# Kernel tuning notes

Measured on AMD Instinct MI355X. Metric: run time of the kernel, lower is better.

Reference implementation:

```python
import jax, jax.numpy as jnp
import numpy as np

D_MODEL = 1024  # scaling uses sqrt(d_model), as in the source


def setup_inputs() -> dict:
    key = jax.random.key(0)
    kx, kq, kk, kv = jax.random.split(key, 4)
    B, N, D, H = 4, 4096, D_MODEL, 128
    X = jax.random.normal(kx, (B, N, D), dtype=jnp.float32)
    # nn.Linear(d_model, d_head, bias=False) weights, stored as [d_model, d_head]
    s = 1.0 / np.sqrt(D)
    Wq = jax.random.normal(kq, (D, H), dtype=jnp.float32) * s
    Wk = jax.random.normal(kk, (D, H), dtype=jnp.float32) * s
    Wv = jax.random.normal(kv, (D, H), dtype=jnp.float32) * s
    return {"X": X, "Wq": Wq, "Wk": Wk, "Wv": Wv}


def reference(X, Wq, Wk, Wv):
    # Q, K, V: [B, N, H]
    Q = jnp.einsum("bnd,dh->bnh", X, Wq)
    K = jnp.einsum("bnd,dh->bnh", X, Wk)
    V = jnp.einsum("bnd,dh->bnh", X, Wv)
    # Scores: [B, N, N]; source divides by sqrt(d_model) (not sqrt(d_head))
    A = jnp.einsum("bqh,bkh->bqk", Q, K) / jnp.sqrt(jnp.float32(D_MODEL))
    A = jax.nn.softmax(A, axis=-1)
    # Dropout is identity in eval mode (deterministic reference baseline)
    return jnp.einsum("bqk,bkh->bqh", A, V)
```

## Files before the change

### kernel.cpp

```cpp
#include <hip/hip_runtime.h>
#include <stdint.h>

typedef __bf16 bf16_t;
typedef bf16_t bf16x8 __attribute__((ext_vector_type(8)));
typedef float f32x4 __attribute__((ext_vector_type(4)));
typedef float f32x16 __attribute__((ext_vector_type(16)));
typedef unsigned short u16;
typedef unsigned int u32;

#define MFMA16(a, b, c) __builtin_amdgcn_mfma_f32_16x16x32_bf16((a), (b), (c), 0, 0, 0)
#define MFMA32(a, b, c) __builtin_amdgcn_mfma_f32_32x32x16_bf16((a), (b), (c), 0, 0, 0)

#define QSCALE 0.04508422002778633f

__device__ __forceinline__ u16 f2bf(float f) {
  union { float f; unsigned u; } v; v.f = f;
  unsigned r = v.u + 0x7fffu + ((v.u >> 16) & 1u);
  return (u16)(r >> 16);
}

__device__ __forceinline__ float exp2x(float x) {
#if __has_builtin(__builtin_amdgcn_exp2f)
  return __builtin_amdgcn_exp2f(x);
#else
  return exp2f(x);
#endif
}

__device__ __forceinline__ float rcpx(float x) {
#if __has_builtin(__builtin_amdgcn_rcpf)
  return __builtin_amdgcn_rcpf(x);
#else
  return 1.0f / x;
#endif
}

__device__ __forceinline__ void async_cp16(const void* g, void* l) {
  __builtin_amdgcn_global_load_lds(
      (__attribute__((address_space(1))) void*)(void*)g,
      (__attribute__((address_space(3))) void*)l, 16, 0, 0);
}

__device__ __forceinline__ u32 cvtpk(float lo, float hi) {
  u32 r;
  asm("v_cvt_pk_bf16_f32 %0, %1, %2" : "=v"(r) : "v"(lo), "v"(hi));
  return r;
}
__device__ __forceinline__ void pl32swap(u32& a, u32& b) {
  asm volatile("v_permlane32_swap_b32 %0, %1" : "+v"(a), "+v"(b));
}

__global__ __launch_bounds__(256) void pack_w_k(const float* __restrict__ Wq,
                                                const float* __restrict__ Wk,
                                                const float* __restrict__ Wv,
                                                u16* __restrict__ wp) {
  int t = blockIdx.x * 256 + threadIdx.x;
  int mat = t >> 14;
  int rr = t & 16383;
  int frag = rr >> 6, lane = rr & 63;
  int nt = frag >> 5, kc = frag & 31;
  const float* W = (mat == 0) ? Wq : ((mat == 1) ? Wk : Wv);
  int k0 = kc * 32 + ((lane >> 4) << 3);
  int col = nt * 16 + (lane & 15);
  union { u16 h[8]; uint4 q; } u_;
#pragma unroll
  for (int j = 0; j < 8; ++j) u_.h[j] = f2bf(W[(size_t)(k0 + j) * 128 + col]);
  *(uint4*)(wp + (size_t)t * 8) = u_.q;
}

__device__ __forceinline__ void qkv_stage(const char* Xb, char* dst, int m0,
                                          int kc, int tid) {
#pragma unroll
  for (int i = 0; i < 2; ++i) {
    int p = i * 4096 + tid * 16;
    int row = p >> 8, cb = p & 255;
    int ucb = cb ^ ((row & 7) << 4);
    async_cp16(Xb + ((size_t)(m0 + row) * 4096 + (size_t)kc * 256 + ucb),
               dst + p);
  }
}

__global__ __launch_bounds__(256) void qkv_k(const float* __restrict__ X,
                                             const u16* __restrict__ wp,
                                             u16* __restrict__ Qf,
                                             u16* __restrict__ Kf,
                                             u16* __restrict__ Vf) {
  __shared__ __align__(16) char xs[2][8192];
  __shared__ __align__(16) u16 eq[4096];
  __shared__ __align__(16) u16 ek[4096];
  __shared__ __align__(16) u16 ev[4096];
  const int tid = threadIdx.x;
  const int w = tid >> 6, lane = tid & 63;
  const int r16 = lane >> 4, c16 = lane & 15;
  const int l31 = lane & 31, hi = lane >> 5;
  const int m0 = blockIdx.x * 32;
  const char* Xb = (const char*)X;

  f32x4 acc[2][6];
#pragma unroll
  for (int mt = 0; mt < 2; ++mt)
#pragma unroll
    for (int i = 0; i < 6; ++i) acc[mt][i] = (f32x4){0.f, 0.f, 0.f, 0.f};

  qkv_stage(Xb, xs[0], m0, 0, tid);
  qkv_stage(Xb, xs[1], m0, 1, tid);

  for (int kc = 0; kc < 16; ++kc) {
    if (kc + 1 < 16) {
      asm volatile("s_waitcnt vmcnt(2)" ::: "memory");
    } else {
      asm volatile("s_waitcnt vmcnt(0)" ::: "memory");
    }
    __builtin_amdgcn_s_barrier();
    asm volatile("" ::: "memory");

    const char* xb = xs[kc & 1];
    bf16x8 bw[6][2];
#pragma unroll
    for (int i = 0; i < 6; ++i) {
      int t = w + 4 * i;
      int mat = t >> 3, nt = t & 7;
      const u16* bp = wp + (size_t)mat * 131072 +
                      (size_t)((nt * 32 + kc * 2) * 64 + lane) * 8;
      bw[i][0] = *(const bf16x8*)(bp);
      bw[i][1] = *(const bf16x8*)(bp + 512);
    }
    bf16x8 a[2][2];
#pragma unroll
    for (int mt = 0; mt < 2; ++mt)
#pragma unroll
      for (int ks = 0; ks < 2; ++ks) {
        int row = mt * 16 + c16;
        int swz = (row & 7) << 4;
        int cb0 = ks * 128 + r16 * 32;
        f32x4 lo = *(const f32x4*)(xb + row * 256 + (cb0 ^ swz));
        f32x4 hi_ = *(const f32x4*)(xb + row * 256 + ((cb0 + 16) ^ swz));
        union { u32 u[4]; bf16x8 v; } pu;
        pu.u[0] = cvtpk(lo[0], lo[1]);
        pu.u[1] = cvtpk(lo[2], lo[3]);
        pu.u[2] = cvtpk(hi_[0], hi_[1]);
        pu.u[3] = cvtpk(hi_[2], hi_[3]);
        a[mt][ks] = pu.v;
      }
#pragma unroll
    for (int i = 0; i < 6; ++i)
#pragma unroll
      for (int ks = 0; ks < 2; ++ks)
#pragma unroll
        for (int mt = 0; mt < 2; ++mt)
          acc[mt][i] = MFMA16(a[mt][ks], bw[i][ks], acc[mt][i]);

    asm volatile("" ::: "memory");
    __builtin_amdgcn_s_barrier();
    asm volatile("" ::: "memory");
    if (kc + 2 < 16) qkv_stage(Xb, xs[kc & 1], m0, kc + 2, tid);
  }

#pragma unroll
  for (int i = 0; i < 6; ++i) {
    int t = w + 4 * i;
    int mat = t >> 3, nt = t & 7;
#pragma unroll
    for (int mt = 0; mt < 2; ++mt) {
      f32x4 v = acc[mt][i];
      if (mat == 2) {
        int d = nt * 16 + c16;
        int n2 = (mt * 16 + r16 * 4) * 2;
        union { u16 h[4]; uint2 q; } u_;
#pragma unroll
        for (int r = 0; r < 4; ++r) u_.h[r] = f2bf(v[r]);
        *(uint2*)((char*)ev + d * 64 + (n2 ^ ((d & 3) << 4))) = u_.q;
      } else {
        char* tile = (char*)((mat == 0) ? eq : ek);
        float sc = (mat == 0) ? QSCALE : 1.0f;
#pragma unroll
        for (int r = 0; r < 4; ++r) {
          int row = mt * 16 + r16 * 4 + r;
          int cb = (nt * 16 + c16) * 2;
          *(u16*)(tile + row * 256 + (cb ^ ((row & 15) << 4))) = f2bf(v[r] * sc);
        }
      }
    }
  }
  __syncthreads();

  const int batch = m0 >> 12, loc = m0 & 4095;
  const int r32 = loc >> 5;
  const int t64 = loc >> 6, kb0 = (loc & 63) >> 4;
#pragma unroll
  for (int p = 0; p < 2; ++p) {
    int kc = p * 4 + w;
    int cb = (kc * 16 + hi * 8) * 2;
    uint4 q_ = *(const uint4*)((const char*)eq + l31 * 256 + (cb ^ ((l31 & 15) << 4)));
    *(uint4*)(Qf + ((size_t)(batch * 1024 + r32 * 8 + kc) * 64 + lane) * 8) = q_;
    uint4 k_ = *(const uint4*)((const char*)ek + l31 * 256 + (cb ^ ((l31 & 15) << 4)));
    *(uint4*)(Kf + ((size_t)(batch * 1024 + r32 * 8 + kc) * 64 + lane) * 8) = k_;
    int d = w * 32 + l31;
    uint4 v_ = *(const uint4*)((const char*)ev + d * 64 +
                               (((p * 16 + hi * 8) * 2) ^ ((d & 3) << 4)));
    *(uint4*)(Vf + ((size_t)(batch * 1024 + t64 * 16 + (kb0 + p) * 4 + w) * 64 +
                    lane) * 8) = v_;
  }
}

__device__ __forceinline__ void stage16(const char* src, char* dst, int tid) {
#pragma unroll
  for (int i = 0; i < 4; ++i)
    async_cp16(src + i * 4096 + tid * 16, dst + i * 4096 + tid * 16);
}

__global__ __launch_bounds__(256, 3) void attn_k(const u16* __restrict__ Qf,
                                                 const u16* __restrict__ Kf,
                                                 const u16* __restrict__ Vf,
                                                 _Float16* __restrict__ Opart,
                                                 float* __restrict__ Ml,
                                                 int nsplit) {
  __shared__ __align__(16) char smem[49152];
  const int tid = threadIdx.x;
  const int w = tid >> 6, lane = tid & 63;
  const int l31 = lane & 31, hi = lane >> 5;

  const int B = gridDim.x;
  int xcd = blockIdx.x & 7, idx = blockIdx.x >> 3;
  int linear = xcd * (B >> 3) + idx;
  int qt = linear & 31, g = linear >> 5;
  int batch = g / nsplit, split = g - batch * nsplit;
  const int q0 = qt * 128;
  const int t0 = (split * 64) / nsplit;
  const int t1 = ((split + 1) * 64) / nsplit;
  const int T = t1 - t0;

  const char* kfc = (const char*)Kf + (size_t)batch * 1048576 + (size_t)t0 * 16384;
  const char* vfc = (const char*)Vf + (size_t)batch * 1048576 + (size_t)t0 * 16384;
  char* vbuf = smem + 32768;

  bf16x8 qf[8];
  const u16* qbase = Qf + ((size_t)(batch * 1024 + (qt * 4 + w) * 8) * 64 + lane) * 8;
#pragma unroll
  for (int kc = 0; kc < 8; ++kc) qf[kc] = *(const bf16x8*)(qbase + kc * 512);

  f32x16 acc[4];
#pragma unroll
  for (int dt = 0; dt < 4; ++dt)
#pragma unroll
    for (int j = 0; j < 16; ++j) acc[dt][j] = 0.f;
  float lacc[8];
#pragma unroll
  for (int i = 0; i < 8; ++i) lacc[i] = 0.f;

  stage16(kfc, smem, tid);
  stage16(vfc, vbuf, tid);
  if (T > 1) stage16(kfc + 16384, smem + 16384, tid);

  for (int t = 0; t < T; ++t) {
    if (t + 1 < T) {
      asm volatile("s_waitcnt vmcnt(8)" ::: "memory");
    } else {
      asm volatile("s_waitcnt vmcnt(4)" ::: "memory");
    }
    __builtin_amdgcn_s_barrier();
    asm volatile("" ::: "memory");
    const char* kb = smem + (t & 1) * 16384;

    f32x16 sv0 = {};
    __builtin_amdgcn_s_setprio(1);
#pragma unroll
    for (int kc = 0; kc < 8; ++kc) {
      bf16x8 kf = *(const bf16x8*)(kb + kc * 1024 + lane * 16);
      sv0 = MFMA32(kf, qf[kc], sv0);
    }
    __builtin_amdgcn_s_setprio(0);

    f32x16 sv1 = {};
#pragma unroll
    for (int kc = 0; kc < 8; ++kc) {
      bf16x8 kf = *(const bf16x8*)(kb + (8 + kc) * 1024 + lane * 16);
      sv1 = MFMA32(kf, qf[kc], sv1);
    }
#pragma unroll
    for (int i = 0; i < 16; ++i) sv0[i] = exp2x(sv0[i]);
#pragma unroll
    for (int i = 0; i < 8; ++i) lacc[i] += sv0[i] + sv0[i + 8];

    bf16x8 pf[4];
#pragma unroll
    for (int half = 0; half < 2; ++half) {
      const float* p = (const float*)&sv0 + half * 8;
      u32 a0 = cvtpk(p[0], p[1]);
      u32 b0 = cvtpk(p[4], p[5]);
      u32 c0 = cvtpk(p[2], p[3]);
      u32 d0 = cvtpk(p[6], p[7]);
      pl32swap(a0, b0);
      pl32swap(c0, d0);
      union { u32 u[4]; bf16x8 v; } pu;
      pu.u[0] = a0; pu.u[1] = c0; pu.u[2] = b0; pu.u[3] = d0;
      pf[half] = pu.v;
    }

    if (t + 1 < T) {
      asm volatile("s_waitcnt vmcnt(4)" ::: "memory");
    } else {
      asm volatile("s_waitcnt vmcnt(0)" ::: "memory");
    }
    __builtin_amdgcn_s_barrier();
    asm volatile("" ::: "memory");

#pragma unroll
    for (int dt = 0; dt < 4; ++dt) {
#pragma unroll
      for (int ks = 0; ks < 2; ++ks) {
        bf16x8 vf = *(const bf16x8*)(vbuf + (ks * 4 + dt) * 1024 + lane * 16);
        acc[dt] = MFMA32(pf[ks], vf, acc[dt]);
      }
    }
#pragma unroll
    for (int i = 0; i < 16; ++i) sv1[i] = exp2x(sv1[i]);
#pragma unroll
    for (int i = 0; i < 8; ++i) lacc[i] += sv1[i] + sv1[i + 8];
#pragma unroll
    for (int half = 0; half < 2; ++half) {
      const float* p = (const float*)&sv1 + half * 8;
      u32 a0 = cvtpk(p[0], p[1]);
      u32 b0 = cvtpk(p[4], p[5]);
      u32 c0 = cvtpk(p[2], p[3]);
      u32 d0 = cvtpk(p[6], p[7]);
      pl32swap(a0, b0);
      pl32swap(c0, d0);
      union { u32 u[4]; bf16x8 v; } pu;
      pu.u[0] = a0; pu.u[1] = c0; pu.u[2] = b0; pu.u[3] = d0;
      pf[2 + half] = pu.v;
    }

    __builtin_amdgcn_s_setprio(1);
#pragma unroll
    for (int dt = 0; dt < 4; ++dt) {
#pragma unroll
      for (int ks = 2; ks < 4; ++ks) {
        bf16x8 vf = *(const bf16x8*)(vbuf + (ks * 4 + dt) * 1024 + lane * 16);
        acc[dt] = MFMA32(pf[ks], vf, acc[dt]);
      }
    }
    __builtin_amdgcn_s_setprio(0);

    asm volatile("" ::: "memory");
    __builtin_amdgcn_s_barrier();
    asm volatile("" ::: "memory");

    if (t + 1 < T) stage16(vfc + (size_t)(t + 1) * 16384, vbuf, tid);
    if (t + 2 < T) stage16(kfc + (size_t)(t + 2) * 16384, smem + (t & 1) * 16384, tid);
  }

  float ltot = ((lacc[0] + lacc[1]) + (lacc[2] + lacc[3])) +
               ((lacc[4] + lacc[5]) + (lacc[6] + lacc[7]));
  ltot += __shfl_xor(ltot, 32);

  size_t obase = (size_t)split * 16384 + (size_t)batch * 4096 + q0 + w * 32;
#pragma unroll
  for (int dt = 0; dt < 4; ++dt)
#pragma unroll
    for (int r = 0; r < 16; ++r) {
      int qr = (r & 3) + 8 * (r >> 2) + 4 * hi;
      float lq = __shfl(ltot, qr);
      Opart[(obase + qr) * 128 + dt * 32 + l31] = (_Float16)(acc[dt][r] * rcpx(lq));
    }
  if (lane < 32)
    Ml[(size_t)split * 16384 + (size_t)batch * 4096 + q0 + w * 32 + lane] = ltot;
}

template <int S>
__global__ __launch_bounds__(256) void reduce_k(const _Float16* __restrict__ Op,
                                                const float* __restrict__ Ml,
                                                float* __restrict__ Out) {
  int t = blockIdx.x * 256 + threadIdx.x;
  int q = t >> 4, d8 = (t & 15) << 3;
  float ls[S];
  float L = 0.f;
#pragma unroll
  for (int s = 0; s < S; ++s) {
    ls[s] = Ml[(size_t)s * 16384 + q];
    L += ls[s];
  }
  float o[8] = {0.f, 0.f, 0.f, 0.f, 0.f, 0.f, 0.f, 0.f};
#pragma unroll
  for (int s = 0; s < S; ++s) {
    union { uint4 u; _Float16 h[8]; } pv;
    pv.u = *(const uint4*)(Op + ((size_t)s * 16384 + q) * 128 + d8);
#pragma unroll
    for (int j = 0; j < 8; ++j) o[j] += (float)pv.h[j] * ls[s];
  }
  float inv = rcpx(L);
  float4 r0 = {o[0] * inv, o[1] * inv, o[2] * inv, o[3] * inv};
  float4 r1 = {o[4] * inv, o[5] * inv, o[6] * inv, o[7] * inv};
  *(float4*)(Out + (size_t)q * 128 + d8) = r0;
  *(float4*)(Out + (size_t)q * 128 + d8 + 4) = r1;
}

extern "C" void kernel_launch(void* const* d_in, const int* in_sizes, int n_in,
                              void* d_out, int out_size, void* d_ws, size_t ws_size,
                              hipStream_t stream) {
  const float* X  = (const float*)d_in[0];
  const float* Wq = (const float*)d_in[1];
  const float* Wk = (const float*)d_in[2];
  const float* Wv = (const float*)d_in[3];
  float* Out = (float*)d_out;
  char* ws = (char*)d_ws;
  u16* Qf = (u16*)(ws);
  u16* Kf = (u16*)(ws + (4u << 20));
  u16* Vf = (u16*)(ws + (8u << 20));
  u16* Wp = (u16*)(ws + (12u << 20));
  _Float16* Opart = (_Float16*)(ws + (13u << 20));

  int S = (ws_size >= (13ull << 20) + 6ull * (4194304ull + 65536ull)) ? 6 : 4;
  float* Ml = (float*)(ws + (13ull << 20) + (size_t)S * 4194304ull);

  pack_w_k<<<dim3(192), dim3(256), 0, stream>>>(Wq, Wk, Wv, Wp);
  qkv_k<<<dim3(512), dim3(256), 0, stream>>>(X, Wp, Qf, Kf, Vf);
  attn_k<<<dim3(128 * S), dim3(256), 0, stream>>>(Qf, Kf, Vf, Opart, Ml, S);
  if (S == 6)
    reduce_k<6><<<dim3(1024), dim3(256), 0, stream>>>(Opart, Ml, Out);
  else
    reduce_k<4><<<dim3(1024), dim3(256), 0, stream>>>(Opart, Ml, Out);
}
```

Before: 85.47 us.

## Replace split QK/PV software pipeline with single-barrier sequential tile schedule

Reorders the attention inner loop so that each tile waits once for both K and V, computes both 32-wide score blocks, applies exp and packs to bf16, then runs all PV MFMAs together. The V prefetch is now issued before K so that a single vmcnt wait covers both. This drops one barrier per iteration and simplifies the schedule. The cost is that the interleaving of exp/convert work with the PV MFMAs is lost, which may reduce overlap between the VALU and the matrix units.

Result: no change. 83.85 us (-1.9%).

```diff
diff --git a/kernel.cpp b/kernel.cpp
--- a/kernel.cpp
+++ b/kernel.cpp
@@ -248,55 +248,11 @@
 #pragma unroll
   for (int i = 0; i < 8; ++i) lacc[i] = 0.f;
 
+  stage16(vfc, vbuf, tid);
   stage16(kfc, smem, tid);
-  stage16(vfc, vbuf, tid);
   if (T > 1) stage16(kfc + 16384, smem + 16384, tid);
 
   for (int t = 0; t < T; ++t) {
-    if (t + 1 < T) {
-      asm volatile("s_waitcnt vmcnt(8)" ::: "memory");
-    } else {
-      asm volatile("s_waitcnt vmcnt(4)" ::: "memory");
-    }
-    __builtin_amdgcn_s_barrier();
-    asm volatile("" ::: "memory");
-    const char* kb = smem + (t & 1) * 16384;
-
-    f32x16 sv0 = {};
-    __builtin_amdgcn_s_setprio(1);
-#pragma unroll
-    for (int kc = 0; kc < 8; ++kc) {
-      bf16x8 kf = *(const bf16x8*)(kb + kc * 1024 + lane * 16);
-      sv0 = MFMA32(kf, qf[kc], sv0);
-    }
-    __builtin_amdgcn_s_setprio(0);
-
-    f32x16 sv1 = {};
-#pragma unroll
-    for (int kc = 0; kc < 8; ++kc) {
-      bf16x8 kf = *(const bf16x8*)(kb + (8 + kc) * 1024 + lane * 16);
-      sv1 = MFMA32(kf, qf[kc], sv1);
-    }
-#pragma unroll
-    for (int i = 0; i < 16; ++i) sv0[i] = exp2x(sv0[i]);
-#pragma unroll
-    for (int i = 0; i < 8; ++i) lacc[i] += sv0[i] + sv0[i + 8];
-
-    bf16x8 pf[4];
-#pragma unroll
-    for (int half = 0; half < 2; ++half) {
-      const float* p = (const float*)&sv0 + half * 8;
-      u32 a0 = cvtpk(p[0], p[1]);
-      u32 b0 = cvtpk(p[4], p[5]);
-      u32 c0 = cvtpk(p[2], p[3]);
-      u32 d0 = cvtpk(p[6], p[7]);
-      pl32swap(a0, b0);
-      pl32swap(c0, d0);
-      union { u32 u[4]; bf16x8 v; } pu;
-      pu.u[0] = a0; pu.u[1] = c0; pu.u[2] = b0; pu.u[3] = d0;
-      pf[half] = pu.v;
-    }
-
     if (t + 1 < T) {
       asm volatile("s_waitcnt vmcnt(4)" ::: "memory");
     } else {
@@ -304,38 +260,52 @@
     }
     __builtin_amdgcn_s_barrier();
     asm volatile("" ::: "memory");
-
+    const char* kb = smem + (t & 1) * 16384;
+
+    f32x16 sv[2];
+    __builtin_amdgcn_s_setprio(1);
+#pragma unroll
+    for (int nt = 0; nt < 2; ++nt) {
+      f32x16 s = {};
+#pragma unroll
+      for (int kc = 0; kc < 8; ++kc) {
+        bf16x8 kf = *(const bf16x8*)(kb + (nt * 8 + kc) * 1024 + lane * 16);
+        s = MFMA32(kf, qf[kc], s);
+      }
+      sv[nt] = s;
+    }
+    __builtin_amdgcn_s_setprio(0);
+
+#pragma unroll
+    for (int nt = 0; nt < 2; ++nt)
+#pragma unroll
+      for (int i = 0; i < 16; ++i) sv[nt][i] = exp2x(sv[nt][i]);
+#pragma unroll
+    for (int i = 0; i < 8; ++i)
+      lacc[i] += (sv[0][i] + sv[0][i + 8]) + (sv[1][i] + sv[1][i + 8]);
+
+    bf16x8 pf[4];
+#pragma unroll
+    for (int nt = 0; nt < 2; ++nt)
+#pragma unroll
+      for (int half = 0; half < 2; ++half) {
+        const float* p = (const float*)&sv[nt] + half * 8;
+        u32 a0 = cvtpk(p[0], p[1]);
+        u32 b0 = cvtpk(p[4], p[5]);
+        u32 c0 = cvtpk(p[2], p[3]);
+        u32 d0 = cvtpk(p[6], p[7]);
+        pl32swap(a0, b0);
+        pl32swap(c0, d0);
+        union { u32 u[4]; bf16x8 v; } pu;
+        pu.u[0] = a0; pu.u[1] = c0; pu.u[2] = b0; pu.u[3] = d0;
+        pf[nt * 2 + half] = pu.v;
+      }
+
+    __builtin_amdgcn_s_setprio(1);
 #pragma unroll
     for (int dt = 0; dt < 4; ++dt) {
 #pragma unroll
-      for (int ks = 0; ks < 2; ++ks) {
-        bf16x8 vf = *(const bf16x8*)(vbuf + (ks * 4 + dt) * 1024 + lane * 16);
-        acc[dt] = MFMA32(pf[ks], vf, acc[dt]);
-      }
-    }
-#pragma unroll
-    for (int i = 0; i < 16; ++i) sv1[i] = exp2x(sv1[i]);
-#pragma unroll
-    for (int i = 0; i < 8; ++i) lacc[i] += sv1[i] + sv1[i + 8];
-#pragma unroll
-    for (int half = 0; half < 2; ++half) {
-      const float* p = (const float*)&sv1 + half * 8;
-      u32 a0 = cvtpk(p[0], p[1]);
-      u32 b0 = cvtpk(p[4], p[5]);
-      u32 c0 = cvtpk(p[2], p[3]);
-      u32 d0 = cvtpk(p[6], p[7]);
-      pl32swap(a0, b0);
-      pl32swap(c0, d0);
-      union { u32 u[4]; bf16x8 v; } pu;
-      pu.u[0] = a0; pu.u[1] = c0; pu.u[2] = b0; pu.u[3] = d0;
-      pf[2 + half] = pu.v;
-    }
-
-    __builtin_amdgcn_s_setprio(1);
-#pragma unroll
-    for (int dt = 0; dt < 4; ++dt) {
-#pragma unroll
-      for (int ks = 2; ks < 4; ++ks) {
+      for (int ks = 0; ks < 4; ++ks) {
         bf16x8 vf = *(const bf16x8*)(vbuf + (ks * 4 + dt) * 1024 + lane * 16);
         acc[dt] = MFMA32(pf[ks], vf, acc[dt]);
       }
```
